# Optimization experiments

Hardware: AMD Instinct MI355X
Metric: run time of the kernel (lower is better)

The kernel has to match this reference:

```python
import jax, jax.numpy as jnp
import numpy as np

H = W = 2048
NUM_SPREADS = 100
SPREAD = 1                      # spread_size -> kernel 3x3, padding 1
MIN_T = 1e-4                    # min_transmission
THR = 0.05                      # update_threshold
COIN_P = 0.5                    # coin_toss_probability
KS = 1 + 2 * SPREAD


def _maxpool(x):
    # MaxPool2d(kernel=3, stride=1, padding=1) on a 2-D map
    return jax.lax.reduce_window(x, -jnp.inf, jax.lax.max,
                                 (KS, KS), (1, 1), [(SPREAD, SPREAD), (SPREAD, SPREAD)])


def setup_inputs() -> dict:
    key = jax.random.key(0)
    k1, k2, k3 = jax.random.split(key, 3)
    seed = (jax.random.uniform(k1, (H, W)) > 0.999).astype(jnp.float32)
    habitat = jax.random.uniform(k2, (H, W), dtype=jnp.float32)
    goodness = jax.random.uniform(k3, (H, W), dtype=jnp.float32)  # terrain parameter
    return {"seed": seed, "habitat": habitat, "goodness": goodness}


def reference(seed, habitat, goodness):
    rng = jax.random.key(42)
    x0 = seed * habitat * goodness

    def step(carry, i):
        x, empty, done = carry
        k1, k2 = jax.random.split(jax.random.fold_in(rng, i))
        xx = x
        y = x * (1.0 - MIN_T + MIN_T * jax.random.uniform(k1, x.shape, x.dtype))
        y = _maxpool(y)
        y = y * (jax.random.uniform(k2, x.shape, x.dtype) > COIN_P)
        y = y * goodness
        delta = y - xx
        y = y * (delta > THR)
        x_new = jnp.maximum(y, xx)
        empty_new = jnp.where(jnp.sum(delta) == 0, empty + 1, jnp.int32(0))
        # emulate the early `break`: once done, carry state through unchanged
        x_out = jnp.where(done, xx, x_new)
        empty_out = jnp.where(done, empty, empty_new)
        done_out = done | (empty_out > 4)
        return (x_out, empty_out, done_out), None

    init = (x0, jnp.int32(0), jnp.bool_(False))
    (x, _, _), _ = jax.lax.scan(step, init, jnp.arange(NUM_SPREADS))
    return x
```

## Files before the change

kernel.cpp:

```cpp
#include <hip/hip_runtime.h>
#include <stdint.h>


#define HH 2048
#define WW 2048
#define NPIX (HH * WW)
#define SD 64
#define OT 32
#define HALO 16
#define K_MAX 16
#define NB (WW / OT)
#define NTILE (NB * NB)

__host__ __device__ __forceinline__ void tf2x32(uint32_t k0, uint32_t k1,
                                                uint32_t c0, uint32_t c1,
                                                uint32_t* o0, uint32_t* o1) {
  uint32_t ks2 = k0 ^ k1 ^ 0x1BD11BDAu;
  uint32_t x0 = c0 + k0, x1 = c1 + k1;
#define TFR(r) do { x0 += x1; x1 = (x1 << (r)) | (x1 >> (32 - (r))); x1 ^= x0; } while (0);
  TFR(13) TFR(15) TFR(26) TFR(6)
  x0 += k1; x1 += ks2 + 1u;
  TFR(17) TFR(29) TFR(16) TFR(24)
  x0 += ks2; x1 += k0 + 2u;
  TFR(13) TFR(15) TFR(26) TFR(6)
  x0 += k0; x1 += k1 + 3u;
  TFR(17) TFR(29) TFR(16) TFR(24)
  x0 += k1; x1 += ks2 + 4u;
  TFR(13) TFR(15) TFR(26) TFR(6)
  x0 += ks2; x1 += k0 + 5u;
#undef TFR
  *o0 = x0; *o1 = x1;
}

__device__ __forceinline__ float uniform01(uint32_t ka, uint32_t kb, uint32_t p) {
  uint32_t o0, o1;
  tf2x32(ka, kb, 0u, p, &o0, &o1);
  uint32_t bits = o0 ^ o1;
  return __uint_as_float((bits >> 9) | 0x3F800000u) - 1.0f;
}

__device__ __forceinline__ unsigned long long dil1(unsigned long long m) {
  return m | (m << 1) | (m >> 1);
}
__device__ __forceinline__ unsigned long long rmask(int lo, int hi) {
  return (~0ULL >> (63 - (hi - lo))) << lo;
}

struct Keys {
  uint32_t a0[K_MAX], a1[K_MAX], b0[K_MAX], b1[K_MAX];
  int K;
};

__global__ void k_init(const float* __restrict__ seed,
                       const float* __restrict__ hab,
                       const float* __restrict__ good,
                       float* __restrict__ x,
                       unsigned char* __restrict__ st) {
  int p = blockIdx.x * blockDim.x + threadIdx.x;
  if (p >= NPIX) return;
  x[p] = __fmul_rn(__fmul_rn(seed[p], hab[p]), good[p]);
  if (p < NTILE) st[p] = 1;
}

__global__ __launch_bounds__(256) void k_fused(const float* __restrict__ xin,
                                               const float* __restrict__ good,
                                               float* __restrict__ xout,
                                               const unsigned char* __restrict__ st_in,
                                               unsigned char* __restrict__ st_out,
                                               Keys kk) {
  __shared__ float xs[SD * SD];
  __shared__ float ts[SD * SD];
  __shared__ unsigned long long fm[SD];
  __shared__ unsigned long long cm[SD];
  __shared__ unsigned int s_flr[2];
  __shared__ unsigned int s_crw[2];
  __shared__ int s_skip;

  const int tid = threadIdx.x;
  const int wv = tid >> 6, ln = tid & 63;
  const int bx = blockIdx.x, by = blockIdx.y;
  const int tix = by * NB + bx;
  const int r0b = by * OT, c0b = bx * OT;
  const int r0g = r0b - HALO, c0g = c0b - HALO;
  const bool top = (by == 0), bot = (by == NB - 1);
  const bool lef = (bx == 0), rig = (bx == NB - 1);
  const bool edge = top || bot || lef || rig;

  {
    bool act = false;
    if (tid < 9) {
      int dy = tid / 3 - 1, dx = tid % 3 - 1;
      int ny = by + dy, nx = bx + dx;
      if (ny >= 0 && ny < NB && nx >= 0 && nx < NB)
        act = st_in[ny * NB + nx] != 0;
    }
    unsigned long long b = __ballot(act);
    if (tid == 0) s_skip = (b == 0ULL);
    __syncthreads();
  }
  if (s_skip) {
    int r = tid >> 3, c4 = tid & 7;
    int off = (r0b + r) * WW + c0b + 4 * c4;
    *(float4*)(xout + off) = *(const float4*)(xin + off);
    if (tid == 0) st_out[tix] = 0;
    return;
  }

  if (!edge) {
#pragma unroll
    for (int k = 0; k < 4; ++k) {
      int q = tid + 256 * k;
      int sr = q >> 4, c4 = q & 15;
      ((float4*)xs)[q] =
          *(const float4*)(xin + (r0g + sr) * WW + c0g + 4 * c4);
    }
  } else {
    for (int idx = tid; idx < SD * SD; idx += 256) {
      int sr = idx >> 6, sc = idx & 63;
      int gr = r0g + sr; gr = gr < 0 ? 0 : (gr > HH - 1 ? HH - 1 : gr);
      int gc = c0g + sc; gc = gc < 0 ? 0 : (gc > WW - 1 ? WW - 1 : gc);
      xs[idx] = xin[gr * WW + gc];
    }
  }
  if (tid < SD) fm[tid] = 0ULL;
  if (tid < 2) { s_flr[tid] = 0u; s_crw[tid] = 0u; }
  __syncthreads();

  int broke = 0;
  for (int s = 0; s < kk.K; ++s) {
    const int rlo = top ? HALO : s + 1;
    const int rhi = bot ? HALO + OT - 1 : SD - 2 - s;
    const int clo = lef ? HALO : s + 1;
    const int chi = rig ? HALO + OT - 1 : SD - 2 - s;
    const unsigned long long colw = rmask(clo, chi);
    const unsigned long long rowsrect = rmask(rlo, rhi);
    const unsigned long long crw_prev =
        s_crw[0] | ((unsigned long long)s_crw[1] << 32);

    if (s == 0) {
      for (int r = rlo + wv; r <= rhi; r += 4) {
        float a = xs[((r - 1) << 6) + ln];
        float b = xs[(r << 6) + ln];
        float c = xs[((r + 1) << 6) + ln];
        float vv = fmaxf(fmaxf(a, b), c);
        float hl = __shfl(vv, ln - 1);
        float hr = __shfl(vv, ln + 1);
        float M = fmaxf(fmaxf(hl, vv), hr);
        bool flag = false;
        if ((colw >> ln) & 1ULL) {
          float xv = b;
          if (__fsub_rn(M, xv) > 0.05f) {
            float g = good[(r0g + r) * WW + (c0g + ln)];
            if (__fsub_rn(__fmul_rn(M, g), xv) > 0.05f) flag = true;
          }
        }
        unsigned long long f = __ballot(flag) & colw;
        if (ln == 0) {
          fm[r] = f;
          if (f) atomicOr(&s_flr[r >> 5], 1u << (r & 31));
        }
      }
    } else {
      unsigned long long arows = dil1(crw_prev) & rowsrect;
      int idx = 0;
      unsigned long long mrows = arows;
      while (mrows) {
        int r = __builtin_ctzll(mrows); mrows &= mrows - 1;
        if (((idx++) & 3) != wv) continue;
        unsigned long long cn = 0ULL;
        if ((crw_prev >> (r - 1)) & 1ULL) cn |= cm[r - 1];
        if ((crw_prev >> r) & 1ULL) cn |= cm[r];
        if ((crw_prev >> (r + 1)) & 1ULL) cn |= cm[r + 1];
        unsigned long long d = dil1(cn) & colw;
        if (!d) continue;
        float a = xs[((r - 1) << 6) + ln];
        float b = xs[(r << 6) + ln];
        float c = xs[((r + 1) << 6) + ln];
        float vv = fmaxf(fmaxf(a, b), c);
        float hl = __shfl(vv, ln - 1);
        float hr = __shfl(vv, ln + 1);
        float M = fmaxf(fmaxf(hl, vv), hr);
        bool flag = false;
        if ((d >> ln) & 1ULL) {
          float xv = b;
          if (__fsub_rn(M, xv) > 0.05f) {
            float g = good[(r0g + r) * WW + (c0g + ln)];
            if (__fsub_rn(__fmul_rn(M, g), xv) > 0.05f) flag = true;
          }
        }
        unsigned long long f = (fm[r] & ~d) | (__ballot(flag) & d);
        if (ln == 0) {
          fm[r] = f;
          if (f) atomicOr(&s_flr[r >> 5], 1u << (r & 31));
          else   atomicAnd(&s_flr[r >> 5], ~(1u << (r & 31)));
        }
      }
    }
    __syncthreads();

    const unsigned long long flr =
        s_flr[0] | ((unsigned long long)s_flr[1] << 32);
    if (!(flr & rowsrect)) { broke = 1; break; }

    if (tid < 2) s_crw[tid] = 0u;
    {
      unsigned long long jrows = dil1(flr) & rmask(rlo - 1, rhi + 1);
      int idx = 0;
      unsigned long long mrows = jrows;
      while (mrows) {
        int r = __builtin_ctzll(mrows); mrows &= mrows - 1;
        if (((idx++) & 3) != wv) continue;
        unsigned long long fu = 0ULL;
        if (r - 1 >= rlo && r - 1 <= rhi) fu |= fm[r - 1];
        if (r     >= rlo && r     <= rhi) fu |= fm[r];
        if (r + 1 >= rlo && r + 1 <= rhi) fu |= fm[r + 1];
        fu &= colw;
        if (!fu) continue;
        unsigned long long need = dil1(fu);
        if ((need >> ln) & 1ULL) {
          float xv = xs[(r << 6) + ln];
          float tv = 0.0f;
          if (xv != 0.0f) {
            int gr = r0g + r;  gr = gr < 0 ? 0 : (gr > HH - 1 ? HH - 1 : gr);
            int gc = c0g + ln; gc = gc < 0 ? 0 : (gc > WW - 1 ? WW - 1 : gc);
            float u = uniform01(kk.a0[s], kk.a1[s], (uint32_t)(gr * WW + gc));
            float s1 = __fadd_rn((float)(1.0 - 1e-4), __fmul_rn(1e-4f, u));
            tv = __fmul_rn(xv, s1);
          }
          ts[(r << 6) + ln] = tv;
        }
      }
    }
    __syncthreads();

    {
      unsigned long long brows = flr & rowsrect;
      int idx = 0;
      unsigned long long mrows = brows;
      while (mrows) {
        int r = __builtin_ctzll(mrows); mrows &= mrows - 1;
        if (((idx++) & 3) != wv) continue;
        unsigned long long wf = fm[r] & colw;
        if (!wf) continue;
        float t0 = ts[((r - 1) << 6) + ln];
        float t1 = ts[(r << 6) + ln];
        float t2 = ts[((r + 1) << 6) + ln];
        float vt = fmaxf(fmaxf(t0, t1), t2);
        float hl = __shfl(vt, ln - 1);
        float hr = __shfl(vt, ln + 1);
        float m = fmaxf(fmaxf(hl, vt), hr);
        bool ok = false;
        float v = 0.0f;
        if ((wf >> ln) & 1ULL) {
          int gp = (r0g + r) * WW + (c0g + ln);
          float xv = xs[(r << 6) + ln];
          v = __fmul_rn(m, good[gp]);
          if (__fsub_rn(v, xv) > 0.05f) {
            float u2 = uniform01(kk.b0[s], kk.b1[s], (uint32_t)gp);
            ok = (u2 > 0.5f);
          }
        }
        unsigned long long bal = __ballot(ok);
        if (ok) xs[(r << 6) + ln] = v;
        if (bal && ln == 0) {
          cm[r] = bal;
          atomicOr(&s_crw[r >> 5], 1u << (r & 31));
        }
      }
    }
    __syncthreads();

    if (edge) {
      unsigned long long crw =
          s_crw[0] | ((unsigned long long)s_crw[1] << 32);
      if (crw) {
        if (top && tid < SD) xs[(15 << 6) + tid] = xs[(16 << 6) + tid];
        if (bot && tid < SD) xs[(48 << 6) + tid] = xs[(47 << 6) + tid];
        __syncthreads();
        if (lef && tid < SD) xs[(tid << 6) + 15] = xs[(tid << 6) + 16];
        if (rig && tid < SD) xs[(tid << 6) + 48] = xs[(tid << 6) + 47];
        __syncthreads();
      }
    }
  }

  if (tid == 0) st_out[tix] = broke ? 0 : 1;

  {
    int r = tid >> 3, c4 = tid & 7;
    *(float4*)(xout + (r0b + r) * WW + c0b + 4 * c4) =
        *(const float4*)(xs + ((r + HALO) << 6) + HALO + 4 * c4);
  }
}

extern "C" void kernel_launch(void* const* d_in, const int* in_sizes, int n_in,
                              void* d_out, int out_size, void* d_ws, size_t ws_size,
                              hipStream_t stream) {
  const float* seed = (const float*)d_in[0];
  const float* hab  = (const float*)d_in[1];
  const float* good = (const float*)d_in[2];
  float* bufA = (float*)d_out;
  float* bufB = (float*)d_ws;
  unsigned char* stA = (unsigned char*)d_ws + (16u << 20);
  unsigned char* stB = stA + NTILE;

  k_init<<<dim3(NPIX / 256), dim3(256), 0, stream>>>(seed, hab, good, bufB, stA);

  float* cur = bufB;
  unsigned char* stIn = stA; unsigned char* stOut = stB;
  dim3 grd(NB, NB), blk(256);
  for (int base = 0; base < 100; base += K_MAX) {
    Keys kk;
    kk.K = (100 - base < K_MAX) ? (100 - base) : K_MAX;
    for (int s = 0; s < kk.K; ++s) {
      uint32_t f0, f1;
      tf2x32(0u, 42u, 0u, (uint32_t)(base + s), &f0, &f1);
      tf2x32(f0, f1, 0u, 0u, &kk.a0[s], &kk.a1[s]);
      tf2x32(f0, f1, 0u, 1u, &kk.b0[s], &kk.b1[s]);
    }
    float* nxt = (cur == bufB) ? bufA : bufB;
    k_fused<<<grd, blk, 0, stream>>>(cur, good, nxt, stIn, stOut, kk);
    cur = nxt;
    unsigned char* t = stIn; stIn = stOut; stOut = t;
  }
}
```

Measured before the change: 1.278 ms.

## Track per-tile buffer ownership to skip copies of unchanged tiles, prune seed-step rows

Each tile now records in its status byte which ping-pong buffer holds its current data. Tiles that are skipped or that commit no update no longer copy themselves to the other buffer, and neighbours read halos from whichever buffer the status byte points to. A final gather kernel moves tiles still living in bufB into the output buffer. The first-step scan also visits only rows near values above the threshold, using a nonzero-row mask built during the load. This cuts global memory traffic for inactive tiles in exchange for pointer indirection during loads and one extra launch.

```diff
diff --git a/kernel.cpp b/kernel.cpp
--- a/kernel.cpp
+++ b/kernel.cpp
@@ -59,12 +59,23 @@
   int p = blockIdx.x * blockDim.x + threadIdx.x;
   if (p >= NPIX) return;
   x[p] = __fmul_rn(__fmul_rn(seed[p], hab[p]), good[p]);
-  if (p < NTILE) st[p] = 1;
-}
-
-__global__ __launch_bounds__(256) void k_fused(const float* __restrict__ xin,
+  if (p < NTILE) st[p] = 3;
+}
+
+__global__ void k_gather(const float* __restrict__ src,
+                         float* __restrict__ dst,
+                         const unsigned char* __restrict__ st) {
+  int tix = blockIdx.x;
+  if (!(st[tix] & 2)) return;
+  int by = tix >> 6, bx = tix & (NB - 1);
+  int r = threadIdx.x >> 3, c4 = threadIdx.x & 7;
+  int off = (by * OT + r) * WW + bx * OT + 4 * c4;
+  *(float4*)(dst + off) = *(const float4*)(src + off);
+}
+
+__global__ __launch_bounds__(256) void k_fused(float* __restrict__ bufA,
+                                               float* __restrict__ bufB,
                                                const float* __restrict__ good,
-                                               float* __restrict__ xout,
                                                const unsigned char* __restrict__ st_in,
                                                unsigned char* __restrict__ st_out,
                                                Keys kk) {
@@ -74,7 +85,9 @@
   __shared__ unsigned long long cm[SD];
   __shared__ unsigned int s_flr[2];
   __shared__ unsigned int s_crw[2];
-  __shared__ int s_skip;
+  __shared__ unsigned int s_nzr[2];
+  __shared__ const float* s_ptr[9];
+  __shared__ int s_skip, s_mystat, s_committed;
 
   const int tid = threadIdx.x;
   const int wv = tid >> 6, ln = tid & 63;
@@ -91,18 +104,21 @@
     if (tid < 9) {
       int dy = tid / 3 - 1, dx = tid % 3 - 1;
       int ny = by + dy, nx = bx + dx;
-      if (ny >= 0 && ny < NB && nx >= 0 && nx < NB)
-        act = st_in[ny * NB + nx] != 0;
+      unsigned char stv = 0;
+      if (ny >= 0 && ny < NB && nx >= 0 && nx < NB) stv = st_in[ny * NB + nx];
+      act = (stv & 1) != 0;
+      s_ptr[tid] = (stv & 2) ? bufB : bufA;
+      if (tid == 4) s_mystat = stv;
     }
     unsigned long long b = __ballot(act);
     if (tid == 0) s_skip = (b == 0ULL);
+    if (tid < 2) { s_flr[tid] = 0u; s_crw[tid] = 0u; s_nzr[tid] = 0u; }
+    if (tid == 0) s_committed = 0;
     __syncthreads();
   }
+  const int mycur = (s_mystat >> 1) & 1;
   if (s_skip) {
-    int r = tid >> 3, c4 = tid & 7;
-    int off = (r0b + r) * WW + c0b + 4 * c4;
-    *(float4*)(xout + off) = *(const float4*)(xin + off);
-    if (tid == 0) st_out[tix] = 0;
+    if (tid == 0) st_out[tix] = (unsigned char)(mycur << 1);
     return;
   }
 
@@ -111,19 +127,35 @@
     for (int k = 0; k < 4; ++k) {
       int q = tid + 256 * k;
       int sr = q >> 4, c4 = q & 15;
-      ((float4*)xs)[q] =
-          *(const float4*)(xin + (r0g + sr) * WW + c0g + 4 * c4);
+      int gr = r0g + sr, gc = c0g + 4 * c4;
+      const float* base = s_ptr[((gr >> 5) - (by - 1)) * 3 + ((gc >> 5) - (bx - 1))];
+      float4 v = *(const float4*)(base + gr * WW + gc);
+      ((float4*)xs)[q] = v;
+      bool any = v.x > 0.05f || v.y > 0.05f || v.z > 0.05f || v.w > 0.05f;
+      unsigned long long b = __ballot(any);
+      if (ln == 0) {
+        int rr = 4 * wv + 16 * k;
+        unsigned int mb = 0;
+#pragma unroll
+        for (int i = 0; i < 4; ++i)
+          if ((b >> (16 * i)) & 0xFFFFULL) mb |= 1u << i;
+        if (mb) atomicOr(&s_nzr[rr >> 5], mb << (rr & 31));
+      }
     }
   } else {
-    for (int idx = tid; idx < SD * SD; idx += 256) {
+    for (int k = 0; k < 16; ++k) {
+      int idx = tid + 256 * k;
       int sr = idx >> 6, sc = idx & 63;
       int gr = r0g + sr; gr = gr < 0 ? 0 : (gr > HH - 1 ? HH - 1 : gr);
       int gc = c0g + sc; gc = gc < 0 ? 0 : (gc > WW - 1 ? WW - 1 : gc);
-      xs[idx] = xin[gr * WW + gc];
+      const float* base = s_ptr[((gr >> 5) - (by - 1)) * 3 + ((gc >> 5) - (bx - 1))];
+      float xv = base[gr * WW + gc];
+      xs[idx] = xv;
+      unsigned long long b = __ballot(xv > 0.05f);
+      if (ln == 0 && b) atomicOr(&s_nzr[sr >> 5], 1u << (sr & 31));
     }
   }
   if (tid < SD) fm[tid] = 0ULL;
-  if (tid < 2) { s_flr[tid] = 0u; s_crw[tid] = 0u; }
   __syncthreads();
 
   int broke = 0;
@@ -138,7 +170,12 @@
         s_crw[0] | ((unsigned long long)s_crw[1] << 32);
 
     if (s == 0) {
-      for (int r = rlo + wv; r <= rhi; r += 4) {
+      unsigned long long nzr = s_nzr[0] | ((unsigned long long)s_nzr[1] << 32);
+      unsigned long long arows = dil1(nzr) & rowsrect;
+      int idx = 0;
+      while (arows) {
+        int r = __builtin_ctzll(arows); arows &= arows - 1;
+        if (((idx++) & 3) != wv) continue;
         float a = xs[((r - 1) << 6) + ln];
         float b = xs[(r << 6) + ln];
         float c = xs[((r + 1) << 6) + ln];
@@ -163,9 +200,8 @@
     } else {
       unsigned long long arows = dil1(crw_prev) & rowsrect;
       int idx = 0;
-      unsigned long long mrows = arows;
-      while (mrows) {
-        int r = __builtin_ctzll(mrows); mrows &= mrows - 1;
+      while (arows) {
+        int r = __builtin_ctzll(arows); arows &= arows - 1;
         if (((idx++) & 3) != wv) continue;
         unsigned long long cn = 0ULL;
         if ((crw_prev >> (r - 1)) & 1ULL) cn |= cm[r - 1];
@@ -206,9 +242,8 @@
     {
       unsigned long long jrows = dil1(flr) & rmask(rlo - 1, rhi + 1);
       int idx = 0;
-      unsigned long long mrows = jrows;
-      while (mrows) {
-        int r = __builtin_ctzll(mrows); mrows &= mrows - 1;
+      while (jrows) {
+        int r = __builtin_ctzll(jrows); jrows &= jrows - 1;
         if (((idx++) & 3) != wv) continue;
         unsigned long long fu = 0ULL;
         if (r - 1 >= rlo && r - 1 <= rhi) fu |= fm[r - 1];
@@ -236,9 +271,8 @@
     {
       unsigned long long brows = flr & rowsrect;
       int idx = 0;
-      unsigned long long mrows = brows;
-      while (mrows) {
-        int r = __builtin_ctzll(mrows); mrows &= mrows - 1;
+      while (brows) {
+        int r = __builtin_ctzll(brows); brows &= brows - 1;
         if (((idx++) & 3) != wv) continue;
         unsigned long long wf = fm[r] & colw;
         if (!wf) continue;
@@ -265,6 +299,7 @@
         if (bal && ln == 0) {
           cm[r] = bal;
           atomicOr(&s_crw[r >> 5], 1u << (r & 31));
+          s_committed = 1;
         }
       }
     }
@@ -284,13 +319,16 @@
     }
   }
 
-  if (tid == 0) st_out[tix] = broke ? 0 : 1;
-
-  {
+  int newcur = mycur;
+  if (s_committed) {
+    newcur = mycur ^ 1;
+    float* dst = mycur ? bufA : bufB;
     int r = tid >> 3, c4 = tid & 7;
-    *(float4*)(xout + (r0b + r) * WW + c0b + 4 * c4) =
+    *(float4*)(dst + (r0b + r) * WW + c0b + 4 * c4) =
         *(const float4*)(xs + ((r + HALO) << 6) + HALO + 4 * c4);
   }
+  if (tid == 0)
+    st_out[tix] = (unsigned char)((broke ? 0 : 1) | (newcur << 1));
 }
 
 extern "C" void kernel_launch(void* const* d_in, const int* in_sizes, int n_in,
@@ -306,7 +344,6 @@
 
   k_init<<<dim3(NPIX / 256), dim3(256), 0, stream>>>(seed, hab, good, bufB, stA);
 
-  float* cur = bufB;
   unsigned char* stIn = stA; unsigned char* stOut = stB;
   dim3 grd(NB, NB), blk(256);
   for (int base = 0; base < 100; base += K_MAX) {
@@ -318,9 +355,8 @@
       tf2x32(f0, f1, 0u, 0u, &kk.a0[s], &kk.a1[s]);
       tf2x32(f0, f1, 0u, 1u, &kk.b0[s], &kk.b1[s]);
     }
-    float* nxt = (cur == bufB) ? bufA : bufB;
-    k_fused<<<grd, blk, 0, stream>>>(cur, good, nxt, stIn, stOut, kk);
-    cur = nxt;
+    k_fused<<<grd, blk, 0, stream>>>(bufA, bufB, good, stIn, stOut, kk);
     unsigned char* t = stIn; stIn = stOut; stOut = t;
   }
-}
+  k_gather<<<dim3(NTILE), blk, 0, stream>>>(bufB, bufA, stIn);
+}
```

New measurement: 1.298 ms. About the same (+1.5%).
